# Kernel optimization log

Measured on AMD Instinct MI355X. Metric: run time of the kernel, lower is better.

## Reference

```python
import jax, jax.numpy as jnp
import numpy as np
import math

HIDDEN = 256
HEADS = 8
HEAD_DIM = HIDDEN // HEADS
SCALE = math.sqrt(HEAD_DIM)


def setup_inputs() -> dict:
    key = jax.random.key(0)
    ks = jax.random.split(key, 10)
    B, N = 2, 4096
    x = jax.random.normal(ks[0], (B, N, HIDDEN), dtype=jnp.float32)
    pos = jax.random.normal(ks[1], (B, N, 3), dtype=jnp.float32)
    s = 1.0 / math.sqrt(HIDDEN)
    Wq = jax.random.normal(ks[2], (HIDDEN, HIDDEN), dtype=jnp.float32) * s
    bq = jnp.zeros((HIDDEN,), dtype=jnp.float32)
    Wk = jax.random.normal(ks[3], (HIDDEN, HIDDEN), dtype=jnp.float32) * s
    bk = jnp.zeros((HIDDEN,), dtype=jnp.float32)
    Wv = jax.random.normal(ks[4], (HIDDEN, HIDDEN), dtype=jnp.float32) * s
    bv = jnp.zeros((HIDDEN,), dtype=jnp.float32)
    Wo = jax.random.normal(ks[5], (HIDDEN, HIDDEN), dtype=jnp.float32) * s
    bo = jnp.zeros((HIDDEN,), dtype=jnp.float32)
    return {"x": x, "pos": pos, "Wq": Wq, "bq": bq, "Wk": Wk, "bk": bk,
            "Wv": Wv, "bv": bv, "Wo": Wo, "bo": bo}


def _pairwise_dist(pos):
    # Euclidean cdist via the norm trick; clip for numerical safety.
    sq = jnp.sum(pos * pos, axis=-1)  # [B, N]
    d2 = sq[:, :, None] + sq[:, None, :] - 2.0 * jnp.einsum('bic,bjc->bij', pos, pos)
    return jnp.sqrt(jnp.maximum(d2, 0.0))  # [B, N, N]


def reference(x, pos, Wq, bq, Wk, bk, Wv, bv, Wo, bo):
    B, N, _ = x.shape
    # projections -> [B, H, N, Dh]
    def split_heads(t):
        return t.reshape(B, N, HEADS, HEAD_DIM).transpose(0, 2, 1, 3)
    q = split_heads(x @ Wq.T + bq)
    k = split_heads(x @ Wk.T + bk)
    v = split_heads(x @ Wv.T + bv)
    scores = jnp.einsum('bhid,bhjd->bhij', q, k) / SCALE
    dist_bias = -_pairwise_dist(pos) / 10.0  # [B, N, N]
    scores = scores + dist_bias[:, None, :, :]
    attn = jax.nn.softmax(scores, axis=-1)
    out = jnp.einsum('bhij,bhjd->bhid', attn, v)
    out = out.transpose(0, 2, 1, 3).reshape(B, N, HIDDEN)
    return out @ Wo.T + bo
```

## Files before the change

kernel.cpp:

```cpp
#include <hip/hip_runtime.h>

#define BATCH 2
#define SEQ   4096
#define HID   256
#define NHEAD 8
#define DH    32
#define THR_L2 11.5f
#define QSCALE 0.25501639769925074f
#define BIASC (-0.14426950408889634f)

typedef __attribute__((ext_vector_type(8))) _Float16 half8;
typedef __attribute__((ext_vector_type(4))) _Float16 half4;
typedef __attribute__((ext_vector_type(4))) float    f32x4;

__global__ void cvt_f32_f16(const float* __restrict__ src,
                            _Float16* __restrict__ dst, int n) {
    int i = (blockIdx.x * blockDim.x + threadIdx.x) * 4;
    if (i >= n) return;
    f32x4 v = *reinterpret_cast<const f32x4*>(src + i);
    half4 h;
#pragma unroll
    for (int c = 0; c < 4; ++c) h[c] = (_Float16)v[c];
    *reinterpret_cast<half4*>(dst + i) = h;
}

__global__ void cvt_w4(const float* __restrict__ a, const float* __restrict__ b,
                       const float* __restrict__ c, const float* __restrict__ d,
                       _Float16* __restrict__ dst) {
    const float* srcs[4] = {a, b, c, d};
    const float* s = srcs[blockIdx.y];
    const int i = (blockIdx.x * blockDim.x + threadIdx.x) * 4;
    f32x4 v = *reinterpret_cast<const f32x4*>(s + i);
    half4 h;
#pragma unroll
    for (int k = 0; k < 4; ++k) h[k] = (_Float16)v[k];
    *reinterpret_cast<half4*>(dst + (size_t)blockIdx.y * HID * HID + i) = h;
}

__global__ __launch_bounds__(256) void qkv_proj(
    const _Float16* __restrict__ xh, const _Float16* __restrict__ Wh,
    const float* __restrict__ bq, const float* __restrict__ bk,
    const float* __restrict__ bv,
    _Float16* __restrict__ Qh, _Float16* __restrict__ Kh,
    _Float16* __restrict__ Vt)
{
    const int z   = blockIdx.z;
    const int m0  = blockIdx.x * 64;
    const int n0  = blockIdx.y * 64;
    const int tid = threadIdx.x;
    const int w   = tid >> 6, lane = tid & 63;
    const int lr  = lane & 15, lg = lane >> 4;
    const int wr  = (w >> 1) * 32, wc = (w & 1) * 32;

    const _Float16* Wp = Wh + (size_t)z * HID * HID;
    const float* bias = (z == 0) ? bq : (z == 1) ? bk : bv;

    f32x4 acc[2][2] = {};
    const int ar = m0 + wr + lr;
    const int br = n0 + wc + lr;
#pragma unroll
    for (int ks = 0; ks < 8; ++ks) {
        const int ko = ks * 32 + lg * 8;
        half8 a0 = *reinterpret_cast<const half8*>(xh + (size_t)ar * HID + ko);
        half8 a1 = *reinterpret_cast<const half8*>(xh + (size_t)(ar + 16) * HID + ko);
        half8 b0 = *reinterpret_cast<const half8*>(Wp + (size_t)br * HID + ko);
        half8 b1 = *reinterpret_cast<const half8*>(Wp + (size_t)(br + 16) * HID + ko);
        acc[0][0] = __builtin_amdgcn_mfma_f32_16x16x32_f16(a0, b0, acc[0][0], 0, 0, 0);
        acc[0][1] = __builtin_amdgcn_mfma_f32_16x16x32_f16(a0, b1, acc[0][1], 0, 0, 0);
        acc[1][0] = __builtin_amdgcn_mfma_f32_16x16x32_f16(a1, b0, acc[1][0], 0, 0, 0);
        acc[1][1] = __builtin_amdgcn_mfma_f32_16x16x32_f16(a1, b1, acc[1][1], 0, 0, 0);
    }
#pragma unroll
    for (int mf = 0; mf < 2; ++mf)
#pragma unroll
    for (int nf = 0; nf < 2; ++nf)
#pragma unroll
    for (int r = 0; r < 4; ++r) {
        const int m  = m0 + wr + mf * 16 + lg * 4 + r;
        const int o  = n0 + wc + nf * 16 + lr;
        const int bb = m >> 12, nn = m & (SEQ - 1);
        const int hh = o >> 5,  dd = o & (DH - 1);
        float v = acc[mf][nf][r] + bias[o];
        if (z == 0) {
            Qh[(((size_t)(bb * NHEAD + hh) * SEQ) + nn) * DH + dd] =
                (_Float16)(v * QSCALE);
        } else if (z == 1) {
            Kh[(((size_t)(bb * NHEAD + hh) * SEQ) + nn) * DH + dd] = (_Float16)v;
        } else {
            Vt[(((size_t)(bb * NHEAD + hh) * DH) + dd) * SEQ + nn] = (_Float16)v;
        }
    }
}

__global__ __launch_bounds__(512, 4) void attn_kernel(
    const _Float16* __restrict__ Qh, const _Float16* __restrict__ Kh,
    const _Float16* __restrict__ Vt, const float* __restrict__ pos,
    _Float16* __restrict__ AO)
{
    __shared__ __align__(16) float pi4[16][4];
    __shared__ __align__(16) float pj4[256][4];
    __shared__ __align__(16) float biasL[16][260];
    __shared__ __align__(16) _Float16 Pl[NHEAD][16 * 72];
    __shared__ __align__(16) float xposeL[NHEAD][16];

    const int b    = blockIdx.y;
    const int i0   = blockIdx.x * 16;
    const int tid  = threadIdx.x;
    const int w    = tid >> 6;
    const int lane = tid & 63;
    const int lr   = lane & 15, lg = lane >> 4;

    if (tid < 16) {
        const float* p = pos + (size_t)(b * SEQ + i0 + tid) * 3;
        float x = p[0], y = p[1], z = p[2];
        pi4[tid][0] = x; pi4[tid][1] = y; pi4[tid][2] = z;
        pi4[tid][3] = x * x + y * y + z * z;
    }

    const size_t bhh = (size_t)(b * NHEAD + w);
    const _Float16* Qbase = Qh + (bhh * SEQ + i0) * DH;
    const _Float16* Kbase = Kh + bhh * SEQ * DH;
    const _Float16* Vbase = Vt + bhh * DH * SEQ;

    const half8 aq = *reinterpret_cast<const half8*>(Qbase + (size_t)lr * DH + lg * 8);

    f32x4 acc0 = {}, acc1 = {};
    float mrun = -1e30f, lsum = 0.f;

    char* PlW = (char*)&Pl[w][0];

    for (int ch = 0; ch < SEQ / 256; ++ch) {
        __syncthreads();
        if (tid < 256) {
            const float* p = pos + (size_t)(b * SEQ + ch * 256 + tid) * 3;
            float x = p[0], y = p[1], z = p[2];
            pj4[tid][0] = x; pj4[tid][1] = y; pj4[tid][2] = z;
            pj4[tid][3] = x * x + y * y + z * z;
        }
        __syncthreads();
        {
            const int br  = tid & 15;
            const int c0  = (tid >> 4) * 8;
            const float xi = pi4[br][0], yi = pi4[br][1], zi = pi4[br][2], si = pi4[br][3];
            f32x4 o0, o1;
#pragma unroll
            for (int k = 0; k < 8; ++k) {
                const float* pj = &pj4[c0 + k][0];
                float dot = xi * pj[0] + yi * pj[1] + zi * pj[2];
                float d2  = si + pj[3] - 2.f * dot;
                float v   = BIASC * sqrtf(fmaxf(d2, 0.f));
                if (k < 4) o0[k] = v; else o1[k - 4] = v;
            }
            *reinterpret_cast<f32x4*>(&biasL[br][c0])     = o0;
            *reinterpret_cast<f32x4*>(&biasL[br][c0 + 4]) = o1;
        }
        __syncthreads();

        for (int s = 0; s < 4; ++s) {
            const int j0 = ch * 256 + s * 64;

            half8 k8[4];
#pragma unroll
            for (int cf = 0; cf < 4; ++cf)
                k8[cf] = *reinterpret_cast<const half8*>(
                    Kbase + (size_t)(j0 + cf * 16 + lr) * DH + lg * 8);

            f32x4 vv[4];
#pragma unroll
            for (int cf = 0; cf < 4; ++cf) {
                f32x4 zero = {};
                f32x4 sv = __builtin_amdgcn_mfma_f32_16x16x32_f16(k8[cf], aq, zero, 0, 0, 0);
                f32x4 bb = *reinterpret_cast<const f32x4*>(
                    &biasL[lr][s * 64 + cf * 16 + lg * 4]);
                vv[cf] = sv + bb;
            }

            float tmax = vv[0][0];
#pragma unroll
            for (int cf = 0; cf < 4; ++cf)
#pragma unroll
            for (int t = 0; t < 4; ++t) tmax = fmaxf(tmax, vv[cf][t]);

            if (!__all(tmax <= mrun + THR_L2)) {
                float tm = tmax;
                tm = fmaxf(tm, __shfl_xor(tm, 16, 64));
                tm = fmaxf(tm, __shfl_xor(tm, 32, 64));
                const float mnew  = fmaxf(mrun, tm);
                const float alpha = exp2f(mrun - mnew);
                if (lane < 16) xposeL[w][lane] = alpha;
                f32x4 a4 = *reinterpret_cast<const f32x4*>(&xposeL[w][lg * 4]);
                lsum *= alpha;
                mrun = mnew;
                acc0 *= a4;
                acc1 *= a4;
            }

#pragma unroll
            for (int cf = 0; cf < 4; ++cf) {
                f32x4 p;
#pragma unroll
                for (int t = 0; t < 4; ++t) p[t] = exp2f(vv[cf][t] - mrun);
                lsum += (p[0] + p[1]) + (p[2] + p[3]);
                half4 hp;
#pragma unroll
                for (int t = 0; t < 4; ++t) hp[t] = (_Float16)p[t];
                *reinterpret_cast<half4*>(
                    PlW + lr * 144 + (cf * 16 + lg * 4) * 2) = hp;
            }

#pragma unroll
            for (int ks = 0; ks < 2; ++ks) {
                half8 pa = *reinterpret_cast<const half8*>(
                    PlW + lr * 144 + (ks * 32 + lg * 8) * 2);
                half8 bv0 = *reinterpret_cast<const half8*>(
                    Vbase + (size_t)lr * SEQ + j0 + ks * 32 + lg * 8);
                half8 bv1 = *reinterpret_cast<const half8*>(
                    Vbase + (size_t)(16 + lr) * SEQ + j0 + ks * 32 + lg * 8);
                acc0 = __builtin_amdgcn_mfma_f32_16x16x32_f16(pa, bv0, acc0, 0, 0, 0);
                acc1 = __builtin_amdgcn_mfma_f32_16x16x32_f16(pa, bv1, acc1, 0, 0, 0);
            }
        }
    }

    lsum += __shfl_xor(lsum, 16, 64);
    lsum += __shfl_xor(lsum, 32, 64);
    const float inv = 1.f / lsum;
    if (lane < 16) xposeL[w][lane] = inv;
    f32x4 i4 = *reinterpret_cast<const f32x4*>(&xposeL[w][lg * 4]);
#pragma unroll
    for (int t = 0; t < 4; ++t) {
        const size_t row = (size_t)(b * SEQ + i0 + lg * 4 + t) * HID + w * DH;
        AO[row + lr]      = (_Float16)(acc0[t] * i4[t]);
        AO[row + 16 + lr] = (_Float16)(acc1[t] * i4[t]);
    }
}

__global__ __launch_bounds__(256) void out_proj(
    const _Float16* __restrict__ AO, const _Float16* __restrict__ Woh,
    const float* __restrict__ bo, float* __restrict__ out)
{
    const int m0  = blockIdx.x * 64;
    const int n0  = blockIdx.y * 64;
    const int tid = threadIdx.x;
    const int w   = tid >> 6, lane = tid & 63;
    const int lr  = lane & 15, lg = lane >> 4;
    const int wr  = (w >> 1) * 32, wc = (w & 1) * 32;

    f32x4 acc[2][2] = {};
    const int ar = m0 + wr + lr;
    const int br = n0 + wc + lr;
#pragma unroll
    for (int ks = 0; ks < 8; ++ks) {
        const int ko = ks * 32 + lg * 8;
        half8 a0 = *reinterpret_cast<const half8*>(AO + (size_t)ar * HID + ko);
        half8 a1 = *reinterpret_cast<const half8*>(AO + (size_t)(ar + 16) * HID + ko);
        half8 b0 = *reinterpret_cast<const half8*>(Woh + (size_t)br * HID + ko);
        half8 b1 = *reinterpret_cast<const half8*>(Woh + (size_t)(br + 16) * HID + ko);
        acc[0][0] = __builtin_amdgcn_mfma_f32_16x16x32_f16(a0, b0, acc[0][0], 0, 0, 0);
        acc[0][1] = __builtin_amdgcn_mfma_f32_16x16x32_f16(a0, b1, acc[0][1], 0, 0, 0);
        acc[1][0] = __builtin_amdgcn_mfma_f32_16x16x32_f16(a1, b0, acc[1][0], 0, 0, 0);
        acc[1][1] = __builtin_amdgcn_mfma_f32_16x16x32_f16(a1, b1, acc[1][1], 0, 0, 0);
    }
#pragma unroll
    for (int mf = 0; mf < 2; ++mf)
#pragma unroll
    for (int nf = 0; nf < 2; ++nf)
#pragma unroll
    for (int r = 0; r < 4; ++r) {
        const int m = m0 + wr + mf * 16 + lg * 4 + r;
        const int o = n0 + wc + nf * 16 + lr;
        out[(size_t)m * HID + o] = acc[mf][nf][r] + bo[o];
    }
}

extern "C" void kernel_launch(void* const* d_in, const int* in_sizes, int n_in,
                              void* d_out, int out_size, void* d_ws, size_t ws_size,
                              hipStream_t stream)
{
    const float* x   = (const float*)d_in[0];
    const float* pos = (const float*)d_in[1];
    const float* Wq  = (const float*)d_in[2];
    const float* bq  = (const float*)d_in[3];
    const float* Wk  = (const float*)d_in[4];
    const float* bk  = (const float*)d_in[5];
    const float* Wv  = (const float*)d_in[6];
    const float* bv  = (const float*)d_in[7];
    const float* Wo  = (const float*)d_in[8];
    const float* bo  = (const float*)d_in[9];
    float* out = (float*)d_out;

    char* ws = (char*)d_ws;
    _Float16* Qh = (_Float16*)(ws);
    _Float16* Kh = (_Float16*)(ws + (4  << 20));
    _Float16* Vt = (_Float16*)(ws + (8  << 20));
    _Float16* xh = (_Float16*)(ws + (12 << 20));
    _Float16* AO = xh;
    _Float16* Wh = (_Float16*)(ws + (16 << 20));

    const int NX = BATCH * SEQ * HID;
    const int NW = HID * HID;
    cvt_f32_f16<<<NX / 1024, 256, 0, stream>>>(x, xh, NX);
    cvt_w4<<<dim3(NW / 1024, 4), 256, 0, stream>>>(Wq, Wk, Wv, Wo, Wh);

    qkv_proj<<<dim3(BATCH * SEQ / 64, HID / 64, 3), 256, 0, stream>>>(
        xh, Wh, bq, bk, bv, Qh, Kh, Vt);

    attn_kernel<<<dim3(SEQ / 16, BATCH), 512, 0, stream>>>(Qh, Kh, Vt, pos, AO);

    out_proj<<<dim3(BATCH * SEQ / 64, HID / 64), 256, 0, stream>>>(
        AO, Wh + 3 * NW, bo, out);
}
```

Measured before the change: 235.7 us.

## Prefetch K/V tiles, widen bias chunk, fold bias into MFMA accumulator

```diff
diff --git a/kernel.cpp b/kernel.cpp
--- a/kernel.cpp
+++ b/kernel.cpp
@@ -11,7 +11,12 @@
 
 typedef __attribute__((ext_vector_type(8))) _Float16 half8;
 typedef __attribute__((ext_vector_type(4))) _Float16 half4;
+typedef __attribute__((ext_vector_type(2))) __fp16   fp16x2;
 typedef __attribute__((ext_vector_type(4))) float    f32x4;
+
+__device__ __forceinline__ float fast_exp2(float x) {
+    return __builtin_amdgcn_exp2f(x);
+}
 
 __global__ void cvt_f32_f16(const float* __restrict__ src,
                             _Float16* __restrict__ dst, int n) {
@@ -98,8 +103,8 @@
     _Float16* __restrict__ AO)
 {
     __shared__ __align__(16) float pi4[16][4];
-    __shared__ __align__(16) float pj4[256][4];
-    __shared__ __align__(16) float biasL[16][260];
+    __shared__ __align__(16) float pj4[512][4];
+    __shared__ __align__(16) float biasL[16][516];
     __shared__ __align__(16) _Float16 Pl[NHEAD][16 * 72];
     __shared__ __align__(16) float xposeL[NHEAD][16];
 
@@ -119,8 +124,9 @@
 
     const size_t bhh = (size_t)(b * NHEAD + w);
     const _Float16* Qbase = Qh + (bhh * SEQ + i0) * DH;
-    const _Float16* Kbase = Kh + bhh * SEQ * DH;
-    const _Float16* Vbase = Vt + bhh * DH * SEQ;
+    const _Float16* Kl  = Kh + bhh * SEQ * DH + (size_t)lr * DH + lg * 8;
+    const _Float16* Vl0 = Vt + bhh * DH * SEQ + (size_t)lr * SEQ + lg * 8;
+    const _Float16* Vl1 = Vt + bhh * DH * SEQ + (size_t)(16 + lr) * SEQ + lg * 8;
 
     const half8 aq = *reinterpret_cast<const half8*>(Qbase + (size_t)lr * DH + lg * 8);
 
@@ -129,10 +135,10 @@
 
     char* PlW = (char*)&Pl[w][0];
 
-    for (int ch = 0; ch < SEQ / 256; ++ch) {
+    for (int ch = 0; ch < SEQ / 512; ++ch) {
         __syncthreads();
-        if (tid < 256) {
-            const float* p = pos + (size_t)(b * SEQ + ch * 256 + tid) * 3;
+        {
+            const float* p = pos + (size_t)(b * SEQ + ch * 512 + tid) * 3;
             float x = p[0], y = p[1], z = p[2];
             pj4[tid][0] = x; pj4[tid][1] = y; pj4[tid][2] = z;
             pj4[tid][3] = x * x + y * y + z * z;
@@ -140,53 +146,69 @@
         __syncthreads();
         {
             const int br  = tid & 15;
-            const int c0  = (tid >> 4) * 8;
+            const int c0  = (tid >> 4) * 16;
             const float xi = pi4[br][0], yi = pi4[br][1], zi = pi4[br][2], si = pi4[br][3];
-            f32x4 o0, o1;
-#pragma unroll
-            for (int k = 0; k < 8; ++k) {
-                const float* pj = &pj4[c0 + k][0];
-                float dot = xi * pj[0] + yi * pj[1] + zi * pj[2];
-                float d2  = si + pj[3] - 2.f * dot;
-                float v   = BIASC * sqrtf(fmaxf(d2, 0.f));
-                if (k < 4) o0[k] = v; else o1[k - 4] = v;
-            }
-            *reinterpret_cast<f32x4*>(&biasL[br][c0])     = o0;
-            *reinterpret_cast<f32x4*>(&biasL[br][c0 + 4]) = o1;
+#pragma unroll
+            for (int k4 = 0; k4 < 4; ++k4) {
+                f32x4 o;
+#pragma unroll
+                for (int k = 0; k < 4; ++k) {
+                    const float* pj = &pj4[c0 + k4 * 4 + k][0];
+                    float dot = xi * pj[0] + yi * pj[1] + zi * pj[2];
+                    float d2  = si + pj[3] - 2.f * dot;
+                    o[k] = BIASC * sqrtf(fmaxf(d2, 0.f));
+                }
+                *reinterpret_cast<f32x4*>(&biasL[br][c0 + k4 * 4]) = o;
+            }
         }
         __syncthreads();
 
-        for (int s = 0; s < 4; ++s) {
-            const int j0 = ch * 256 + s * 64;
-
-            half8 k8[4];
-#pragma unroll
-            for (int cf = 0; cf < 4; ++cf)
-                k8[cf] = *reinterpret_cast<const half8*>(
-                    Kbase + (size_t)(j0 + cf * 16 + lr) * DH + lg * 8);
+        half8 k8[4];
+#pragma unroll
+        for (int cf = 0; cf < 4; ++cf)
+            k8[cf] = *reinterpret_cast<const half8*>(
+                Kl + (size_t)(ch * 512 + cf * 16) * DH);
+
+#pragma unroll 2
+        for (int s = 0; s < 8; ++s) {
+            const int j0 = ch * 512 + s * 64;
+
+            half8 bva = *reinterpret_cast<const half8*>(Vl0 + j0);
+            half8 bvb = *reinterpret_cast<const half8*>(Vl1 + j0);
+            half8 bvc = *reinterpret_cast<const half8*>(Vl0 + j0 + 32);
+            half8 bvd = *reinterpret_cast<const half8*>(Vl1 + j0 + 32);
 
             f32x4 vv[4];
 #pragma unroll
             for (int cf = 0; cf < 4; ++cf) {
-                f32x4 zero = {};
-                f32x4 sv = __builtin_amdgcn_mfma_f32_16x16x32_f16(k8[cf], aq, zero, 0, 0, 0);
-                f32x4 bb = *reinterpret_cast<const f32x4*>(
+                f32x4 cb = *reinterpret_cast<const f32x4*>(
                     &biasL[lr][s * 64 + cf * 16 + lg * 4]);
-                vv[cf] = sv + bb;
-            }
-
-            float tmax = vv[0][0];
-#pragma unroll
-            for (int cf = 0; cf < 4; ++cf)
-#pragma unroll
-            for (int t = 0; t < 4; ++t) tmax = fmaxf(tmax, vv[cf][t]);
+                vv[cf] = __builtin_amdgcn_mfma_f32_16x16x32_f16(k8[cf], aq, cb, 0, 0, 0);
+            }
+
+            half8 kn[4];
+            if (s < 7) {
+#pragma unroll
+                for (int cf = 0; cf < 4; ++cf)
+                    kn[cf] = *reinterpret_cast<const half8*>(
+                        Kl + (size_t)(j0 + 64 + cf * 16) * DH);
+            }
+
+            float tmax = fmaxf(fmaxf(vv[0][0], vv[0][1]), vv[0][2]);
+            tmax = fmaxf(fmaxf(tmax, vv[0][3]), vv[1][0]);
+            tmax = fmaxf(fmaxf(tmax, vv[1][1]), vv[1][2]);
+            tmax = fmaxf(fmaxf(tmax, vv[1][3]), vv[2][0]);
+            tmax = fmaxf(fmaxf(tmax, vv[2][1]), vv[2][2]);
+            tmax = fmaxf(fmaxf(tmax, vv[2][3]), vv[3][0]);
+            tmax = fmaxf(fmaxf(tmax, vv[3][1]), vv[3][2]);
+            tmax = fmaxf(tmax, vv[3][3]);
 
             if (!__all(tmax <= mrun + THR_L2)) {
                 float tm = tmax;
                 tm = fmaxf(tm, __shfl_xor(tm, 16, 64));
                 tm = fmaxf(tm, __shfl_xor(tm, 32, 64));
                 const float mnew  = fmaxf(mrun, tm);
-                const float alpha = exp2f(mrun - mnew);
+                const float alpha = fast_exp2(mrun - mnew);
                 if (lane < 16) xposeL[w][lane] = alpha;
                 f32x4 a4 = *reinterpret_cast<const f32x4*>(&xposeL[w][lg * 4]);
                 lsum *= alpha;
@@ -197,27 +219,31 @@
 
 #pragma unroll
             for (int cf = 0; cf < 4; ++cf) {
-                f32x4 p;
-#pragma unroll
-                for (int t = 0; t < 4; ++t) p[t] = exp2f(vv[cf][t] - mrun);
-                lsum += (p[0] + p[1]) + (p[2] + p[3]);
-                half4 hp;
-#pragma unroll
-                for (int t = 0; t < 4; ++t) hp[t] = (_Float16)p[t];
-                *reinterpret_cast<half4*>(
-                    PlW + lr * 144 + (cf * 16 + lg * 4) * 2) = hp;
-            }
-
-#pragma unroll
-            for (int ks = 0; ks < 2; ++ks) {
-                half8 pa = *reinterpret_cast<const half8*>(
-                    PlW + lr * 144 + (ks * 32 + lg * 8) * 2);
-                half8 bv0 = *reinterpret_cast<const half8*>(
-                    Vbase + (size_t)lr * SEQ + j0 + ks * 32 + lg * 8);
-                half8 bv1 = *reinterpret_cast<const half8*>(
-                    Vbase + (size_t)(16 + lr) * SEQ + j0 + ks * 32 + lg * 8);
-                acc0 = __builtin_amdgcn_mfma_f32_16x16x32_f16(pa, bv0, acc0, 0, 0, 0);
-                acc1 = __builtin_amdgcn_mfma_f32_16x16x32_f16(pa, bv1, acc1, 0, 0, 0);
+                float p0 = fast_exp2(vv[cf][0] - mrun);
+                float p1 = fast_exp2(vv[cf][1] - mrun);
+                float p2 = fast_exp2(vv[cf][2] - mrun);
+                float p3 = fast_exp2(vv[cf][3] - mrun);
+                lsum += (p0 + p1) + (p2 + p3);
+                fp16x2 ha = __builtin_amdgcn_cvt_pkrtz(p0, p1);
+                fp16x2 hb = __builtin_amdgcn_cvt_pkrtz(p2, p3);
+                unsigned int wlo = __builtin_bit_cast(unsigned int, ha);
+                unsigned int whi = __builtin_bit_cast(unsigned int, hb);
+                unsigned long long wq =
+                    (unsigned long long)wlo | ((unsigned long long)whi << 32);
+                *reinterpret_cast<unsigned long long*>(
+                    PlW + lr * 144 + (cf * 16 + lg * 4) * 2) = wq;
+            }
+
+            half8 pa0 = *reinterpret_cast<const half8*>(PlW + lr * 144 + (lg * 8) * 2);
+            half8 pa1 = *reinterpret_cast<const half8*>(PlW + lr * 144 + (32 + lg * 8) * 2);
+            acc0 = __builtin_amdgcn_mfma_f32_16x16x32_f16(pa0, bva, acc0, 0, 0, 0);
+            acc1 = __builtin_amdgcn_mfma_f32_16x16x32_f16(pa0, bvb, acc1, 0, 0, 0);
+            acc0 = __builtin_amdgcn_mfma_f32_16x16x32_f16(pa1, bvc, acc0, 0, 0, 0);
+            acc1 = __builtin_amdgcn_mfma_f32_16x16x32_f16(pa1, bvd, acc1, 0, 0, 0);
+
+            if (s < 7) {
+#pragma unroll
+                for (int cf = 0; cf < 4; ++cf) k8[cf] = kn[cf];
             }
         }
     }
```

After: 235.7 us. No clear change (-0.0%).
